# Kernel optimization log

Hardware: AMD Instinct MI355X
Metric: run time of the kernel (lower is better)

Reference implementation:

```python
import jax, jax.numpy as jnp
import numpy as np

N = 100000
E = 640000
D = 128


def _sage_conv(x, src, dst, Wp, bp, Wl, bl, Wr):
    # project=True: project + relu source features before aggregation
    h = jax.nn.relu(x @ Wp.T + bp)            # [N, D]
    msgs = h[src]                              # [E, D] gather
    summed = jax.ops.segment_sum(msgs, dst, num_segments=N)   # [N, D]
    cnt = jax.ops.segment_sum(jnp.ones((msgs.shape[0],), x.dtype), dst, num_segments=N)
    mean = summed / jnp.maximum(cnt, 1.0)[:, None]
    # lin_l on aggregated neighbors (with bias) + lin_r on root (no bias)
    return mean @ Wl.T + bl + x @ Wr.T


def setup_inputs() -> dict:
    key = jax.random.key(0)
    ks = jax.random.split(key, 16)
    s = 1.0 / np.sqrt(D)
    x = jax.random.normal(ks[0], (N, D), dtype=jnp.float32)
    edge_index = jax.random.randint(ks[1], (2, E), 0, N, dtype=jnp.int64)
    params = {}
    for i, base in enumerate(["conv0", "conv1"]):
        params[base + "_Wp"] = jax.random.uniform(ks[2 + 5 * i], (D, D), jnp.float32, -s, s)
        params[base + "_bp"] = jax.random.uniform(ks[3 + 5 * i], (D,), jnp.float32, -s, s)
        params[base + "_Wl"] = jax.random.uniform(ks[4 + 5 * i], (D, D), jnp.float32, -s, s)
        params[base + "_bl"] = jax.random.uniform(ks[5 + 5 * i], (D,), jnp.float32, -s, s)
        params[base + "_Wr"] = jax.random.uniform(ks[6 + 5 * i], (D, D), jnp.float32, -s, s)
    return {"x": x, "edge_index": edge_index, **params}


def reference(x, edge_index,
              conv0_Wp, conv0_bp, conv0_Wl, conv0_bl, conv0_Wr,
              conv1_Wp, conv1_bp, conv1_Wl, conv1_bl, conv1_Wr):
    src, dst = edge_index[0], edge_index[1]
    h = _sage_conv(x, src, dst, conv0_Wp, conv0_bp, conv0_Wl, conv0_bl, conv0_Wr)
    h = jax.nn.relu(h)
    return _sage_conv(h, src, dst, conv1_Wp, conv1_bp, conv1_Wl, conv1_bl, conv1_Wr)
```

## Files before the change

kernel.cpp:

```cpp
#include <hip/hip_runtime.h>

#define DD 128

typedef _Float16 f16;
typedef __attribute__((ext_vector_type(8))) _Float16 v8h;
typedef __attribute__((ext_vector_type(4))) _Float16 v4h;
typedef __attribute__((ext_vector_type(4))) float f32x4;

static inline int cdiv(int a, int b) { return (a + b - 1) / b; }


__global__ __launch_bounds__(256) void zero_kernel(int* __restrict__ p, int n) {
    int i = blockIdx.x * 256 + threadIdx.x;
    if (i < n) p[i] = 0;
}


__global__ __launch_bounds__(256) void count_kernel(const int* __restrict__ dst, int E,
                                                    int* __restrict__ cnt) {
    int e = blockIdx.x * 256 + threadIdx.x;
    if (e < E) atomicAdd(&cnt[dst[e]], 1);
}

__global__ __launch_bounds__(256) void scan1(const int* __restrict__ cnt, int N,
                                             int* __restrict__ bsum) {
    __shared__ int s[256];
    int i = blockIdx.x * 256 + threadIdx.x;
    s[threadIdx.x] = (i < N) ? cnt[i] : 0;
    __syncthreads();
    for (int off = 128; off > 0; off >>= 1) {
        if (threadIdx.x < off) s[threadIdx.x] += s[threadIdx.x + off];
        __syncthreads();
    }
    if (threadIdx.x == 0) bsum[blockIdx.x] = s[0];
}

__global__ __launch_bounds__(512) void scan2(const int* __restrict__ bsum, int NB,
                                             int* __restrict__ boff) {
    __shared__ int s[512];
    int t = threadIdx.x;
    int v = (t < NB) ? bsum[t] : 0;
    s[t] = v;
    __syncthreads();
    for (int off = 1; off < 512; off <<= 1) {
        int x = (t >= off) ? s[t - off] : 0;
        __syncthreads();
        s[t] += x;
        __syncthreads();
    }
    if (t < NB) boff[t] = s[t] - v;
}

__global__ __launch_bounds__(256) void scan3(const int* __restrict__ cnt,
                                             const int* __restrict__ boff, int N,
                                             int* __restrict__ off) {
    __shared__ int s[256];
    int t = threadIdx.x;
    int i = blockIdx.x * 256 + t;
    int v = (i < N) ? cnt[i] : 0;
    s[t] = v;
    __syncthreads();
    for (int o = 1; o < 256; o <<= 1) {
        int x = (t >= o) ? s[t - o] : 0;
        __syncthreads();
        s[t] += x;
        __syncthreads();
    }
    int excl = s[t] - v + boff[blockIdx.x];
    if (i < N) off[i] = excl;
    if (i == N - 1) off[N] = excl + v;
}

__global__ __launch_bounds__(256) void fill_kernel(const int* __restrict__ src,
                                                   const int* __restrict__ dst, int E,
                                                   const int* __restrict__ off,
                                                   int* __restrict__ cnt,
                                                   int* __restrict__ csr) {
    int e = blockIdx.x * 256 + threadIdx.x;
    if (e < E) {
        int d = dst[e];
        int p = atomicSub(&cnt[d], 1) - 1;
        csr[off[d] + p] = src[e];
    }
}


__global__ __launch_bounds__(256) void cvt_w_kernel(const float* __restrict__ W0,
                                                    const float* __restrict__ W1,
                                                    const float* __restrict__ W2,
                                                    const float* __restrict__ W3,
                                                    const float* __restrict__ W4,
                                                    const float* __restrict__ W5,
                                                    f16* __restrict__ out) {
    int mat = blockIdx.x >> 4;
    const float* W = mat == 0 ? W0 : mat == 1 ? W1 : mat == 2 ? W2
                   : mat == 3 ? W3 : mat == 4 ? W4 : W5;
    int base = (blockIdx.x & 15) * 1024 + threadIdx.x * 4;
    float4 v = *(const float4*)(W + base);
    v4h o;
    o[0] = (f16)v.x; o[1] = (f16)v.y; o[2] = (f16)v.z; o[3] = (f16)v.w;
    *(v4h*)(out + mat * 16384 + base) = o;
}


__global__ __launch_bounds__(256) void aggregate_kernel(const f16* __restrict__ h,
                                                        const int* __restrict__ off,
                                                        const int* __restrict__ csr,
                                                        f16* __restrict__ mean, int N) {
    int n = blockIdx.x * 4 + (threadIdx.x >> 6);
    int l = threadIdx.x & 63;
    int g = l >> 4, c = l & 15;
    if (n >= N) return;
    int s = off[n], e = off[n + 1];
    float acc[8] = {0.f, 0.f, 0.f, 0.f, 0.f, 0.f, 0.f, 0.f};
    for (int base = s; base < e; base += 32) {
        v8h v[8];
        float wgt[8];
#pragma unroll
        for (int u = 0; u < 8; ++u) {
            int i = base + g + u * 4;
            int ic = i < e ? i : (e - 1);
            wgt[u] = (i < e) ? 1.f : 0.f;
            v[u] = *(const v8h*)(h + (size_t)csr[ic] * DD + c * 8);
        }
#pragma unroll
        for (int u = 0; u < 8; ++u)
#pragma unroll
            for (int j = 0; j < 8; ++j) acc[j] = fmaf(wgt[u], (float)v[u][j], acc[j]);
    }
#pragma unroll
    for (int j = 0; j < 8; ++j) {
        acc[j] += __shfl_xor(acc[j], 16);
        acc[j] += __shfl_xor(acc[j], 32);
    }
    int deg = e - s;
    float inv = 1.0f / (float)(deg > 0 ? deg : 1);
    if (g == 0) {
        v8h o;
#pragma unroll
        for (int j = 0; j < 8; ++j) o[j] = (f16)(acc[j] * inv);
        *(v8h*)(mean + (size_t)n * DD + c * 8) = o;
    }
}


__device__ inline void stage_w(const f16* __restrict__ Wg, f16* __restrict__ smem, int t) {
#pragma unroll
    for (int i = 0; i < 8; ++i) {
        int idx16 = i * 256 + t;
        int col = idx16 >> 4, c16 = idx16 & 15;
        int sc = c16 ^ (col & 7);
        uint4 v = *(const uint4*)(Wg + idx16 * 8);
        *(uint4*)(smem + col * DD + sc * 8) = v;
    }
}

__device__ inline v8h read_b(const f16* __restrict__ smem, int ct, int ki, int l) {
    int col = ct * 16 + (l & 15);
    int c16 = ki * 4 + (l >> 4);
    int sc = c16 ^ (col & 7);
    return *(const v8h*)(smem + col * DD + sc * 8);
}

__device__ inline v8h load_frag16(const f16* __restrict__ A, int row, int kb, int M) {
    if (row >= M) {
        v8h z = {};
        return z;
    }
    return *(const v8h*)(A + (size_t)row * DD + kb);
}


template <typename TA, bool WX>
__global__ __launch_bounds__(256) void proj_gemm(const TA* __restrict__ A,
                                                 const f16* __restrict__ W1,
                                                 const float* __restrict__ bias,
                                                 f16* __restrict__ OUT,
                                                 f16* __restrict__ A16, int M) {
    __shared__ f16 WS[DD * DD];
    int t = threadIdx.x, l = t & 63, w = t >> 6;
    int row0 = blockIdx.x * 128 + w * 32;
    int r = l & 15, cg = l >> 4;

    stage_w(W1, WS, t);

    v8h af[2][4];
#pragma unroll
    for (int rt = 0; rt < 2; ++rt) {
        int row = row0 + rt * 16 + r;
#pragma unroll
        for (int ki = 0; ki < 4; ++ki) {
            int kb = ki * 32 + cg * 8;
            if constexpr (sizeof(TA) == 2) {
                af[rt][ki] = load_frag16(A, row, kb, M);
            } else {
                if (row < M) {
                    float4 a = *(const float4*)(A + (size_t)row * DD + kb);
                    float4 b = *(const float4*)(A + (size_t)row * DD + kb + 4);
                    v8h rr;
                    rr[0] = (f16)a.x; rr[1] = (f16)a.y; rr[2] = (f16)a.z; rr[3] = (f16)a.w;
                    rr[4] = (f16)b.x; rr[5] = (f16)b.y; rr[6] = (f16)b.z; rr[7] = (f16)b.w;
                    af[rt][ki] = rr;
                } else {
                    v8h z = {};
                    af[rt][ki] = z;
                }
            }
            if constexpr (WX) {
                if (row < M) *(v8h*)(A16 + (size_t)row * DD + kb) = af[rt][ki];
            }
        }
    }
    __syncthreads();

    f32x4 acc[2][8];
#pragma unroll
    for (int ct = 0; ct < 8; ++ct) {
        float bv = bias[ct * 16 + r];
        f32x4 b4 = {bv, bv, bv, bv};
        acc[0][ct] = b4;
        acc[1][ct] = b4;
    }

#pragma unroll
    for (int ct = 0; ct < 8; ++ct)
#pragma unroll
        for (int ki = 0; ki < 4; ++ki) {
            v8h b = read_b(WS, ct, ki, l);
            acc[0][ct] = __builtin_amdgcn_mfma_f32_16x16x32_f16(af[0][ki], b, acc[0][ct], 0, 0, 0);
            acc[1][ct] = __builtin_amdgcn_mfma_f32_16x16x32_f16(af[1][ki], b, acc[1][ct], 0, 0, 0);
        }

#pragma unroll
    for (int rt = 0; rt < 2; ++rt)
#pragma unroll
        for (int ct = 0; ct < 8; ++ct)
#pragma unroll
            for (int j = 0; j < 4; ++j) {
                int row = row0 + rt * 16 + cg * 4 + j;
                if (row < M)
                    OUT[(size_t)row * DD + ct * 16 + r] = (f16)fmaxf(acc[rt][ct][j], 0.f);
            }
}


template <typename TO, bool RELU>
__global__ __launch_bounds__(256) void dual_gemm(const f16* __restrict__ A,
                                                 const f16* __restrict__ Wl,
                                                 const float* __restrict__ bias,
                                                 const f16* __restrict__ B,
                                                 const f16* __restrict__ Wr,
                                                 TO* __restrict__ OUT, int M) {
    __shared__ f16 WS[DD * DD];
    int t = threadIdx.x, l = t & 63, w = t >> 6;
    int row0 = blockIdx.x * 128 + w * 32;
    int r = l & 15, cg = l >> 4;

    stage_w(Wl, WS, t);

    v8h afA[2][4], afB[2][4];
#pragma unroll
    for (int rt = 0; rt < 2; ++rt)
#pragma unroll
        for (int ki = 0; ki < 4; ++ki) {
            int row = row0 + rt * 16 + r, kb = ki * 32 + cg * 8;
            afA[rt][ki] = load_frag16(A, row, kb, M);
            afB[rt][ki] = load_frag16(B, row, kb, M);
        }
    __syncthreads();

    f32x4 acc[2][8];
#pragma unroll
    for (int ct = 0; ct < 8; ++ct) {
        float bv = bias[ct * 16 + r];
        f32x4 b4 = {bv, bv, bv, bv};
        acc[0][ct] = b4;
        acc[1][ct] = b4;
    }

#pragma unroll
    for (int ct = 0; ct < 8; ++ct)
#pragma unroll
        for (int ki = 0; ki < 4; ++ki) {
            v8h b = read_b(WS, ct, ki, l);
            acc[0][ct] = __builtin_amdgcn_mfma_f32_16x16x32_f16(afA[0][ki], b, acc[0][ct], 0, 0, 0);
            acc[1][ct] = __builtin_amdgcn_mfma_f32_16x16x32_f16(afA[1][ki], b, acc[1][ct], 0, 0, 0);
        }

    __syncthreads();
    stage_w(Wr, WS, t);
    __syncthreads();

#pragma unroll
    for (int ct = 0; ct < 8; ++ct)
#pragma unroll
        for (int ki = 0; ki < 4; ++ki) {
            v8h b = read_b(WS, ct, ki, l);
            acc[0][ct] = __builtin_amdgcn_mfma_f32_16x16x32_f16(afB[0][ki], b, acc[0][ct], 0, 0, 0);
            acc[1][ct] = __builtin_amdgcn_mfma_f32_16x16x32_f16(afB[1][ki], b, acc[1][ct], 0, 0, 0);
        }

#pragma unroll
    for (int rt = 0; rt < 2; ++rt)
#pragma unroll
        for (int ct = 0; ct < 8; ++ct)
#pragma unroll
            for (int j = 0; j < 4; ++j) {
                int row = row0 + rt * 16 + cg * 4 + j;
                if (row < M) {
                    float v = acc[rt][ct][j];
                    if (RELU) v = fmaxf(v, 0.f);
                    OUT[(size_t)row * DD + ct * 16 + r] = (TO)v;
                }
            }
}


extern "C" void kernel_launch(void* const* d_in, const int* in_sizes, int n_in,
                              void* d_out, int out_size, void* d_ws, size_t ws_size,
                              hipStream_t stream) {
    const float* x = (const float*)d_in[0];
    const int* ei = (const int*)d_in[1];
    const float* Wp0 = (const float*)d_in[2];
    const float* bp0 = (const float*)d_in[3];
    const float* Wl0 = (const float*)d_in[4];
    const float* bl0 = (const float*)d_in[5];
    const float* Wr0 = (const float*)d_in[6];
    const float* Wp1 = (const float*)d_in[7];
    const float* bp1 = (const float*)d_in[8];
    const float* Wl1 = (const float*)d_in[9];
    const float* bl1 = (const float*)d_in[10];
    const float* Wr1 = (const float*)d_in[11];

    int N = in_sizes[0] / DD;
    int E = in_sizes[1] / 2;
    const int* src = ei;
    const int* dst = ei + E;

    char* ws = (char*)d_ws;
    size_t o = 0;
    auto alloc = [&](size_t bytes) {
        size_t r = o;
        o = (o + bytes + 255) & ~(size_t)255;
        return r;
    };
    f16* w16 = (f16*)(ws + alloc((size_t)6 * DD * DD * 2));
    int* cnt = (int*)(ws + alloc((size_t)N * 4));
    int* off = (int*)(ws + alloc((size_t)(N + 1) * 4));
    int NB = cdiv(N, 256);
    int* bsum = (int*)(ws + alloc((size_t)NB * 4));
    int* boff = (int*)(ws + alloc((size_t)NB * 4));
    int* csr = (int*)(ws + alloc((size_t)E * 4));
    f16* mean = (f16*)(ws + alloc((size_t)N * DD * 2));
    f16* y1 = (f16*)(ws + alloc((size_t)N * DD * 2));
    f16* h = (f16*)d_out;
    f16* x16 = (f16*)((char*)d_out + (size_t)N * DD * 2);
    (void)ws_size;

    zero_kernel<<<NB, 256, 0, stream>>>(cnt, N);
    count_kernel<<<cdiv(E, 256), 256, 0, stream>>>(dst, E, cnt);
    scan1<<<NB, 256, 0, stream>>>(cnt, N, bsum);
    scan2<<<1, 512, 0, stream>>>(bsum, NB, boff);
    scan3<<<NB, 256, 0, stream>>>(cnt, boff, N, off);
    fill_kernel<<<cdiv(E, 256), 256, 0, stream>>>(src, dst, E, off, cnt, csr);

    cvt_w_kernel<<<96, 256, 0, stream>>>(Wp0, Wl0, Wr0, Wp1, Wl1, Wr1, w16);
    const f16* wp0 = w16 + 0 * 16384;
    const f16* wl0 = w16 + 1 * 16384;
    const f16* wr0 = w16 + 2 * 16384;
    const f16* wp1 = w16 + 3 * 16384;
    const f16* wl1 = w16 + 4 * 16384;
    const f16* wr1 = w16 + 5 * 16384;

    int GB = cdiv(N, 128);
    proj_gemm<float, true><<<GB, 256, 0, stream>>>(x, wp0, bp0, h, x16, N);
    aggregate_kernel<<<cdiv(N, 4), 256, 0, stream>>>(h, off, csr, mean, N);
    dual_gemm<f16, true><<<GB, 256, 0, stream>>>(mean, wl0, bl0, x16, wr0, y1, N);
    proj_gemm<f16, false><<<GB, 256, 0, stream>>>(y1, wp1, bp1, h, nullptr, N);
    aggregate_kernel<<<cdiv(N, 4), 256, 0, stream>>>(h, off, csr, mean, N);
    dual_gemm<float, false><<<GB, 256, 0, stream>>>(mean, wl1, bl1, y1, wr1, (float*)d_out, N);
}
```

Baseline: 280.4 us.

## Use grid-stride aggregation with simple per-edge loop and separate x conversion kernel

```diff
diff --git a/kernel.cpp b/kernel.cpp
--- a/kernel.cpp
+++ b/kernel.cpp
@@ -102,44 +102,48 @@
     *(v4h*)(out + mat * 16384 + base) = o;
 }
 
+__global__ __launch_bounds__(256) void cvt_x_kernel(const float* __restrict__ x,
+                                                    f16* __restrict__ out, int n8) {
+    int i = blockIdx.x * 256 + threadIdx.x;
+    if (i >= n8) return;
+    float4 a = *(const float4*)(x + (size_t)i * 8);
+    float4 b = *(const float4*)(x + (size_t)i * 8 + 4);
+    v8h r;
+    r[0] = (f16)a.x; r[1] = (f16)a.y; r[2] = (f16)a.z; r[3] = (f16)a.w;
+    r[4] = (f16)b.x; r[5] = (f16)b.y; r[6] = (f16)b.z; r[7] = (f16)b.w;
+    *(v8h*)(out + (size_t)i * 8) = r;
+}
+
 
 __global__ __launch_bounds__(256) void aggregate_kernel(const f16* __restrict__ h,
                                                         const int* __restrict__ off,
                                                         const int* __restrict__ csr,
                                                         f16* __restrict__ mean, int N) {
-    int n = blockIdx.x * 4 + (threadIdx.x >> 6);
     int l = threadIdx.x & 63;
     int g = l >> 4, c = l & 15;
-    if (n >= N) return;
-    int s = off[n], e = off[n + 1];
-    float acc[8] = {0.f, 0.f, 0.f, 0.f, 0.f, 0.f, 0.f, 0.f};
-    for (int base = s; base < e; base += 32) {
-        v8h v[8];
-        float wgt[8];
-#pragma unroll
-        for (int u = 0; u < 8; ++u) {
-            int i = base + g + u * 4;
-            int ic = i < e ? i : (e - 1);
-            wgt[u] = (i < e) ? 1.f : 0.f;
-            v[u] = *(const v8h*)(h + (size_t)csr[ic] * DD + c * 8);
-        }
-#pragma unroll
-        for (int u = 0; u < 8; ++u)
-#pragma unroll
-            for (int j = 0; j < 8; ++j) acc[j] = fmaf(wgt[u], (float)v[u][j], acc[j]);
-    }
-#pragma unroll
-    for (int j = 0; j < 8; ++j) {
-        acc[j] += __shfl_xor(acc[j], 16);
-        acc[j] += __shfl_xor(acc[j], 32);
-    }
-    int deg = e - s;
-    float inv = 1.0f / (float)(deg > 0 ? deg : 1);
-    if (g == 0) {
-        v8h o;
-#pragma unroll
-        for (int j = 0; j < 8; ++j) o[j] = (f16)(acc[j] * inv);
-        *(v8h*)(mean + (size_t)n * DD + c * 8) = o;
+    int stride = gridDim.x * 4;
+    for (int n = blockIdx.x * 4 + (threadIdx.x >> 6); n < N; n += stride) {
+        int s = off[n], e = off[n + 1];
+        float acc[8] = {0.f, 0.f, 0.f, 0.f, 0.f, 0.f, 0.f, 0.f};
+        for (int i = s + g; i < e; i += 4) {
+            int idx = csr[i];
+            v8h v = *(const v8h*)(h + (size_t)idx * DD + c * 8);
+#pragma unroll
+            for (int j = 0; j < 8; ++j) acc[j] += (float)v[j];
+        }
+#pragma unroll
+        for (int j = 0; j < 8; ++j) {
+            acc[j] += __shfl_xor(acc[j], 16);
+            acc[j] += __shfl_xor(acc[j], 32);
+        }
+        int deg = e - s;
+        float inv = 1.0f / (float)(deg > 0 ? deg : 1);
+        if (g == 0) {
+            v8h o;
+#pragma unroll
+            for (int j = 0; j < 8; ++j) o[j] = (f16)(acc[j] * inv);
+            *(v8h*)(mean + (size_t)n * DD + c * 8) = o;
+        }
     }
 }
 
@@ -171,12 +175,10 @@
 }
 
 
-template <typename TA, bool WX>
-__global__ __launch_bounds__(256) void proj_gemm(const TA* __restrict__ A,
+__global__ __launch_bounds__(256) void proj_gemm(const f16* __restrict__ A,
                                                  const f16* __restrict__ W1,
                                                  const float* __restrict__ bias,
-                                                 f16* __restrict__ OUT,
-                                                 f16* __restrict__ A16, int M) {
+                                                 f16* __restrict__ OUT, int M) {
     __shared__ f16 WS[DD * DD];
     int t = threadIdx.x, l = t & 63, w = t >> 6;
     int row0 = blockIdx.x * 128 + w * 32;
@@ -186,31 +188,10 @@
 
     v8h af[2][4];
 #pragma unroll
-    for (int rt = 0; rt < 2; ++rt) {
-        int row = row0 + rt * 16 + r;
-#pragma unroll
-        for (int ki = 0; ki < 4; ++ki) {
-            int kb = ki * 32 + cg * 8;
-            if constexpr (sizeof(TA) == 2) {
-                af[rt][ki] = load_frag16(A, row, kb, M);
-            } else {
-                if (row < M) {
-                    float4 a = *(const float4*)(A + (size_t)row * DD + kb);
-                    float4 b = *(const float4*)(A + (size_t)row * DD + kb + 4);
-                    v8h rr;
-                    rr[0] = (f16)a.x; rr[1] = (f16)a.y; rr[2] = (f16)a.z; rr[3] = (f16)a.w;
-                    rr[4] = (f16)b.x; rr[5] = (f16)b.y; rr[6] = (f16)b.z; rr[7] = (f16)b.w;
-                    af[rt][ki] = rr;
-                } else {
-                    v8h z = {};
-                    af[rt][ki] = z;
-                }
-            }
-            if constexpr (WX) {
-                if (row < M) *(v8h*)(A16 + (size_t)row * DD + kb) = af[rt][ki];
-            }
-        }
-    }
+    for (int rt = 0; rt < 2; ++rt)
+#pragma unroll
+        for (int ki = 0; ki < 4; ++ki)
+            af[rt][ki] = load_frag16(A, row0 + rt * 16 + r, ki * 32 + cg * 8, M);
     __syncthreads();
 
     f32x4 acc[2][8];
@@ -372,11 +353,14 @@
     const f16* wl1 = w16 + 4 * 16384;
     const f16* wr1 = w16 + 5 * 16384;
 
+    cvt_x_kernel<<<cdiv(N * DD / 8, 256), 256, 0, stream>>>(x, x16, N * DD / 8);
+
     int GB = cdiv(N, 128);
-    proj_gemm<float, true><<<GB, 256, 0, stream>>>(x, wp0, bp0, h, x16, N);
-    aggregate_kernel<<<cdiv(N, 4), 256, 0, stream>>>(h, off, csr, mean, N);
+    const int AGG_GRID = 2048;
+    proj_gemm<<<GB, 256, 0, stream>>>(x16, wp0, bp0, h, N);
+    aggregate_kernel<<<AGG_GRID, 256, 0, stream>>>(h, off, csr, mean, N);
     dual_gemm<f16, true><<<GB, 256, 0, stream>>>(mean, wl0, bl0, x16, wr0, y1, N);
-    proj_gemm<f16, false><<<GB, 256, 0, stream>>>(y1, wp1, bp1, h, nullptr, N);
-    aggregate_kernel<<<cdiv(N, 4), 256, 0, stream>>>(h, off, csr, mean, N);
+    proj_gemm<<<GB, 256, 0, stream>>>(y1, wp1, bp1, h, N);
+    aggregate_kernel<<<AGG_GRID, 256, 0, stream>>>(h, off, csr, mean, N);
     dual_gemm<float, false><<<GB, 256, 0, stream>>>(mean, wl1, bl1, y1, wr1, (float*)d_out, N);
 }
```

After: 243.9 us. 13.0% less time.
